# Kernel optimization log

Measured on AMD Instinct MI355X. Metric: run time of the kernel, lower is better.

The kernel has to match this reference:

```python
import jax, jax.numpy as jnp
import numpy as np

N, F, H, D, E, G = 50000, 64, 4, 64, 800000, 64
NEG_SLOPE = 0.2


def setup_inputs() -> dict:
    key = jax.random.key(0)
    ks = jax.random.split(key, 10)
    return {
        "x": jax.random.normal(ks[0], (N, F), jnp.float32),
        "mask": jax.random.uniform(ks[1], (N, F), jnp.float32),
        "edge_index": jax.random.randint(ks[2], (2, E), 0, N, jnp.int64),
        "batch_idx": jnp.sort(jax.random.randint(ks[3], (N,), 0, G, jnp.int64)),
        "W_gat": jax.random.normal(ks[4], (H * D, F), jnp.float32) * 0.05,
        "att_src": jax.random.normal(ks[5], (H, D), jnp.float32) * 0.05,
        "att_dst": jax.random.normal(ks[6], (H, D), jnp.float32) * 0.05,
        "bias_gat": jax.random.normal(ks[7], (H * D,), jnp.float32) * 0.05,
        "W_lin": jax.random.normal(ks[8], (D, H * D), jnp.float32) * 0.05,
        "b_lin": jax.random.normal(ks[9], (D,), jnp.float32) * 0.05,
    }


def reference(x, mask, edge_index, batch_idx, W_gat, att_src, att_dst, bias_gat, W_lin, b_lin):
    n = x.shape[0]
    row, col = edge_index[0], edge_index[1]

    # ---- get_mask(mask, edge_index, hops=1): scatter_add(mask[col] -> row), threshold
    m = jax.ops.segment_sum(mask[col], row, num_segments=n)
    m = (m > 0).astype(x.dtype)  # [N, F]

    # ---- GATConv(x, edge_index): add self loops (PyG default)
    loop = jnp.arange(n, dtype=edge_index.dtype)
    src = jnp.concatenate([edge_index[0], loop])  # source j
    dst = jnp.concatenate([edge_index[1], loop])  # target i

    xw = (x @ W_gat.T).reshape(n, H, D)  # per-head projection [N,H,D]
    a_s = jnp.einsum("nhd,hd->nh", xw, att_src)  # [N,H]
    a_d = jnp.einsum("nhd,hd->nh", xw, att_dst)
    e = jax.nn.leaky_relu(a_s[src] + a_d[dst], NEG_SLOPE)  # [E+N, H]

    # segment softmax over incoming edges of each destination node
    emax = jax.ops.segment_max(e, dst, num_segments=n)  # [N,H]
    ex = jnp.exp(e - emax[dst])
    denom = jax.ops.segment_sum(ex, dst, num_segments=n)
    alpha = ex / (denom[dst] + 1e-16)  # [E+N, H]

    out = jax.ops.segment_sum(alpha[:, :, None] * xw[src], dst, num_segments=n)
    out = out.reshape(n, H * D) + bias_gat  # concat heads + bias

    # ---- mask expand to heads and fuse: x = linear(x * mask)
    mexp = jnp.broadcast_to(m[:, None, :], (n, H, F)).reshape(n, H * F)
    out = (out * mexp) @ W_lin.T + b_lin  # [N, D]

    # ---- GraphSizeNorm: divide by sqrt(#nodes in each graph)
    deg = jax.ops.segment_sum(jnp.ones((n,), x.dtype), batch_idx, num_segments=G)
    inv_sqrt = jnp.where(deg > 0, deg, 1.0) ** -0.5
    out = out * inv_sqrt[batch_idx][:, None]
    return out
```

## Files before the change

kernel.cpp:

```cpp
#include <hip/hip_runtime.h>
#include <cstdint>
#include <math.h>

constexpr float NEG_SLOPE = 0.2f;

__device__ __forceinline__ float lrelu(float v) { return v > 0.0f ? v : NEG_SLOPE * v; }

__device__ __forceinline__ unsigned short f2bf(float f) {
    uint32_t u = __float_as_uint(f);
    uint32_t r = (u + 0x7fffu + ((u >> 16) & 1u)) >> 16;
    return (unsigned short)r;
}
__device__ __forceinline__ float bf2f(unsigned short v) { return __uint_as_float((uint32_t)v << 16); }
__device__ __forceinline__ float bflo(uint32_t v) { return __uint_as_float(v << 16); }
__device__ __forceinline__ float bfhi(uint32_t v) { return __uint_as_float(v & 0xffff0000u); }

typedef short bf16x8 __attribute__((ext_vector_type(8)));
typedef float f32x4 __attribute__((ext_vector_type(4)));

__global__ void k_init(const float* __restrict__ mask,
                       unsigned long long* __restrict__ mbits,
                       unsigned long long* __restrict__ magg,
                       int* __restrict__ deg, int* __restrict__ startg, int N)
{
    if (blockIdx.x == 0 && threadIdx.x < 64) startg[threadIdx.x] = N;
    int wid  = (blockIdx.x * blockDim.x + threadIdx.x) >> 6;
    int lane = threadIdx.x & 63;
    if (wid >= N) return;
    float v = mask[(size_t)wid * 64 + lane];
    unsigned long long b = __ballot(v > 0.0f);
    if (lane == 0) { mbits[wid] = b; magg[wid] = 0ULL; deg[wid] = 0; }
}

__global__ void k_edge_prep(const int* __restrict__ ei,
                            const unsigned long long* __restrict__ mbits,
                            unsigned long long* __restrict__ magg,
                            int* __restrict__ deg, int E)
{
    int e = blockIdx.x * blockDim.x + threadIdx.x;
    if (e >= E) return;
    int r = ei[e];
    int c = ei[E + e];
    unsigned long long b = mbits[c];
    if ((magg[r] & b) != b) atomicOr(magg + r, b);
    atomicAdd(deg + c, 1);
}

__launch_bounds__(256)
__global__ void k_att2(const float* __restrict__ x, const float* __restrict__ Wg,
                       const float* __restrict__ att_s, const float* __restrict__ att_d,
                       float* __restrict__ a_s, float* __restrict__ a_d, int N)
{
    __shared__ float vs_l[256];
    __shared__ float vd_l[256];
    int tid = threadIdx.x;
    {
        int h = tid >> 6, k = tid & 63;
        float s = 0.f, d = 0.f;
        for (int dd = 0; dd < 64; ++dd) {
            float w = Wg[(size_t)(h * 64 + dd) * 64 + k];
            s += w * att_s[h * 64 + dd];
            d += w * att_d[h * 64 + dd];
        }
        vs_l[tid] = s; vd_l[tid] = d;
    }
    __syncthreads();
    int i = blockIdx.x * 256 + tid;
    if (i >= N) return;
    const float4* xr = (const float4*)(x + (size_t)i * 64);
    float s0=0,s1=0,s2=0,s3=0, d0=0,d1=0,d2=0,d3=0;
    #pragma unroll
    for (int q = 0; q < 16; ++q) {
        float4 xv = xr[q];
        float4 a0 = *(const float4*)&vs_l[4*q];
        float4 a1 = *(const float4*)&vs_l[64 + 4*q];
        float4 a2 = *(const float4*)&vs_l[128 + 4*q];
        float4 a3 = *(const float4*)&vs_l[192 + 4*q];
        float4 c0 = *(const float4*)&vd_l[4*q];
        float4 c1 = *(const float4*)&vd_l[64 + 4*q];
        float4 c2 = *(const float4*)&vd_l[128 + 4*q];
        float4 c3 = *(const float4*)&vd_l[192 + 4*q];
        s0 += xv.x*a0.x + xv.y*a0.y + xv.z*a0.z + xv.w*a0.w;
        s1 += xv.x*a1.x + xv.y*a1.y + xv.z*a1.z + xv.w*a1.w;
        s2 += xv.x*a2.x + xv.y*a2.y + xv.z*a2.z + xv.w*a2.w;
        s3 += xv.x*a3.x + xv.y*a3.y + xv.z*a3.z + xv.w*a3.w;
        d0 += xv.x*c0.x + xv.y*c0.y + xv.z*c0.z + xv.w*c0.w;
        d1 += xv.x*c1.x + xv.y*c1.y + xv.z*c1.z + xv.w*c1.w;
        d2 += xv.x*c2.x + xv.y*c2.y + xv.z*c2.z + xv.w*c2.w;
        d3 += xv.x*c3.x + xv.y*c3.y + xv.z*c3.z + xv.w*c3.w;
    }
    *(float4*)&a_s[(size_t)i * 4] = make_float4(s0, s1, s2, s3);
    *(float4*)&a_d[(size_t)i * 4] = make_float4(d0, d1, d2, d3);
}

__launch_bounds__(256)
__global__ void k_gemm1m(const float* __restrict__ x, const float* __restrict__ Wg,
                         const int* __restrict__ batch_idx,
                         uint32_t* __restrict__ xwp, int* __restrict__ startg, int N)
{
    __shared__ __align__(16) uint32_t AsH[2048];
    __shared__ __align__(16) uint32_t AsL[2048];
    __shared__ __align__(16) uint32_t BsH[8192];
    const int tid = threadIdx.x;
    const int r0  = blockIdx.x * 64;

    for (int idx = tid; idx < 2048; idx += 256) {
        int r = idx >> 5, k2 = idx & 31;
        float2 v = make_float2(0.f, 0.f);
        if (r0 + r < N) v = *(const float2*)&x[(size_t)(r0 + r) * 64 + 2 * k2];
        unsigned short h0 = f2bf(v.x), h1 = f2bf(v.y);
        unsigned short l0 = f2bf(v.x - bf2f(h0)), l1 = f2bf(v.y - bf2f(h1));
        int di = (r * 32 + k2) ^ ((r & 7) << 2);
        AsH[di] = (uint32_t)h0 | ((uint32_t)h1 << 16);
        AsL[di] = (uint32_t)l0 | ((uint32_t)l1 << 16);
    }
    for (int idx = tid; idx < 8192; idx += 256) {
        int c = idx >> 5, k2 = idx & 31;
        float2 v = *(const float2*)&Wg[(size_t)c * 64 + 2 * k2];
        int di = (c * 32 + k2) ^ ((c & 7) << 2);
        BsH[di] = (uint32_t)f2bf(v.x) | ((uint32_t)f2bf(v.y) << 16);
    }
    if (tid < 64 && (r0 + tid) < N) {
        int i = r0 + tid;
        int b = batch_idx[i];
        int pb = (i > 0) ? batch_idx[i - 1] : -1;
        if (b != pb) startg[b] = i;
    }
    __syncthreads();

    const int lane = tid & 63;
    const int wv   = tid >> 6;
    const int rl   = lane & 15;
    const int kg   = lane >> 4;
    const int ct0  = (wv & 1) * 2 + (wv >> 1) * 8;
    const int swz  = (rl & 7) << 2;

    f32x4 acc[4][4];
    #pragma unroll
    for (int r = 0; r < 4; ++r)
        #pragma unroll
        for (int cs = 0; cs < 4; ++cs) acc[r][cs] = (f32x4){0.f, 0.f, 0.f, 0.f};

    #pragma unroll
    for (int ks = 0; ks < 2; ++ks) {
        bf16x8 aH[4], aL[4], bH[4];
        #pragma unroll
        for (int r = 0; r < 4; ++r) {
            int ui = (((r * 16 + rl) * 32) + ks * 16 + kg * 4) ^ swz;
            aH[r] = *(const bf16x8*)&AsH[ui];
            aL[r] = *(const bf16x8*)&AsL[ui];
        }
        #pragma unroll
        for (int cs = 0; cs < 4; ++cs) {
            int ct = ct0 + (cs & 1) + (cs >> 1) * 4;
            int ui = (((ct * 16 + rl) * 32) + ks * 16 + kg * 4) ^ swz;
            bH[cs] = *(const bf16x8*)&BsH[ui];
        }
        #pragma unroll
        for (int r = 0; r < 4; ++r)
            #pragma unroll
            for (int cs = 0; cs < 4; ++cs) {
                acc[r][cs] = __builtin_amdgcn_mfma_f32_16x16x32_bf16(aH[r], bH[cs], acc[r][cs], 0, 0, 0);
                acc[r][cs] = __builtin_amdgcn_mfma_f32_16x16x32_bf16(aL[r], bH[cs], acc[r][cs], 0, 0, 0);
            }
    }

    #pragma unroll
    for (int r = 0; r < 4; ++r) {
        #pragma unroll
        for (int reg = 0; reg < 4; ++reg) {
            int row = r0 + r * 16 + kg * 4 + reg;
            if (row < N) {
                #pragma unroll
                for (int p = 0; p < 2; ++p) {
                    int c_lo = (ct0 + p) * 16 + rl;
                    int wrd  = ((c_lo >> 7) << 6) | (c_lo & 63);
                    uint32_t lo = f2bf(acc[r][p][reg]);
                    uint32_t hi = f2bf(acc[r][p + 2][reg]);
                    xwp[(size_t)row * 128 + wrd] = lo | (hi << 16);
                }
            }
        }
    }
}

__global__ void k_scan1(const int* __restrict__ deg, int* __restrict__ off,
                        int* __restrict__ bsum, int N)
{
    __shared__ int s[256];
    int t = threadIdx.x;
    int i = blockIdx.x * 256 + t;
    int v = (i < N) ? deg[i] : 0;
    s[t] = v; __syncthreads();
    for (int o = 1; o < 256; o <<= 1) {
        int u = (t >= o) ? s[t - o] : 0;
        __syncthreads();
        s[t] += u;
        __syncthreads();
    }
    int incl = s[t];
    if (i < N) off[i] = incl - v;
    if (t == 255) bsum[blockIdx.x] = incl;
}

__global__ void k_scan2(const int* __restrict__ bsum, int* __restrict__ bpre,
                        int* __restrict__ off, const int* __restrict__ startg,
                        float* __restrict__ invs, int NB, int N)
{
    __shared__ int s[256];
    int t = threadIdx.x;
    int v = (t < NB) ? bsum[t] : 0;
    s[t] = v; __syncthreads();
    for (int o = 1; o < 256; o <<= 1) {
        int u = (t >= o) ? s[t - o] : 0;
        __syncthreads();
        s[t] += u;
        __syncthreads();
    }
    if (t < NB) bpre[t] = s[t] - v;
    if (t == 255) off[N] = s[255];
    if (t < 64) {
        int st = startg[t];
        int en = N;
        for (int g2 = t + 1; g2 < 64; ++g2) en = min(en, startg[g2]);
        int d = en - st;
        float dv = (d > 0) ? (float)d : 1.0f;
        invs[t] = 1.0f / sqrtf(dv);
    }
}

__global__ void k_scan3(int* __restrict__ off, int* __restrict__ cursor,
                        const int* __restrict__ bpre, int N)
{
    int i = blockIdx.x * blockDim.x + threadIdx.x;
    if (i >= N) return;
    int v = off[i] + bpre[blockIdx.x];
    off[i] = v;
    cursor[i] = v;
}

__global__ void k_fill(const int* __restrict__ ei, int* __restrict__ cursor,
                       int* __restrict__ csr, int E)
{
    int e = blockIdx.x * blockDim.x + threadIdx.x;
    if (e >= E) return;
    int r = ei[e];
    int c = ei[E + e];
    int pos = atomicAdd(cursor + c, 1);
    csr[pos] = r;
}

__launch_bounds__(256)
__global__ void k_main5(const uint32_t* __restrict__ xwp,
                        const float* __restrict__ a_s,
                        const float* __restrict__ a_d,
                        const int* __restrict__ off,
                        const int* __restrict__ csr,
                        const unsigned long long* __restrict__ magg,
                        const float* __restrict__ bias,
                        float* __restrict__ tb, int N)
{
    __shared__ __align__(16) uint32_t su[4][64];
    __shared__ float2 e01s[4][64];
    __shared__ float2 e23s[4][64];

    const int lane = threadIdx.x & 63;
    const int wv   = threadIdx.x >> 6;
    const int wid  = blockIdx.x * 4 + wv;
    const int nw   = gridDim.x * 4;
    const int hp   = lane >> 5;
    const int d0   = (lane & 31) * 2;

    const uint2* xw2 = (const uint2*)xwp;
    const float2 bsL = *(const float2*)&bias[hp * 128 + d0];
    const float2 bsH = *(const float2*)&bias[hp * 128 + 64 + d0];
    const float2* ep = hp ? e23s[wv] : e01s[wv];

    for (int i = wid; i < N; i += nw) {
        const int beg = off[i], end = off[i + 1];
        const float4 adv = *(const float4*)(a_d + (size_t)i * 4);
        const float4 asv = *(const float4*)(a_s + (size_t)i * 4);
        const float ex0 = __expf(lrelu(asv.x + adv.x));
        const float ex1 = __expf(lrelu(asv.y + adv.y));
        const float ex2 = __expf(lrelu(asv.z + adv.z));
        const float ex3 = __expf(lrelu(asv.w + adv.w));

        const uint2 sv = xw2[(size_t)i * 64 + lane];
        const float wls = hp ? ex2 : ex0;
        const float whs = hp ? ex3 : ex1;
        float accL0 = wls * bflo(sv.x), accH0 = whs * bfhi(sv.x);
        float accL1 = wls * bflo(sv.y), accH1 = whs * bfhi(sv.y);
        float s0 = 0.f, s1 = 0.f, s2 = 0.f, s3 = 0.f;

        for (int kc = beg; kc < end; kc += 64) {
            const int cnt = min(64, end - kc);
            uint32_t sreg = 0; float e0 = 0.f, e1 = 0.f, e2 = 0.f, e3 = 0.f;
            if (lane < cnt) {
                sreg = csr[kc + lane];
                const float4 g = *(const float4*)(a_s + (size_t)sreg * 4);
                e0 = __expf(lrelu(g.x + adv.x));
                e1 = __expf(lrelu(g.y + adv.y));
                e2 = __expf(lrelu(g.z + adv.z));
                e3 = __expf(lrelu(g.w + adv.w));
            }
            s0 += e0; s1 += e1; s2 += e2; s3 += e3;
            su[wv][lane]   = sreg;
            e01s[wv][lane] = make_float2(e0, e1);
            e23s[wv][lane] = make_float2(e2, e3);

            int j = 0;
            for (; j + 4 <= cnt; j += 4) {
                uint4 sq = *(const uint4*)&su[wv][j];
                float2 wA = ep[j], wB = ep[j+1], wC = ep[j+2], wD = ep[j+3];
                uint2 vA = xw2[(size_t)sq.x * 64 + lane];
                uint2 vB = xw2[(size_t)sq.y * 64 + lane];
                uint2 vC = xw2[(size_t)sq.z * 64 + lane];
                uint2 vD = xw2[(size_t)sq.w * 64 + lane];
                accL0 += wA.x * bflo(vA.x); accH0 += wA.y * bfhi(vA.x);
                accL1 += wA.x * bflo(vA.y); accH1 += wA.y * bfhi(vA.y);
                accL0 += wB.x * bflo(vB.x); accH0 += wB.y * bfhi(vB.x);
                accL1 += wB.x * bflo(vB.y); accH1 += wB.y * bfhi(vB.y);
                accL0 += wC.x * bflo(vC.x); accH0 += wC.y * bfhi(vC.x);
                accL1 += wC.x * bflo(vC.y); accH1 += wC.y * bfhi(vC.y);
                accL0 += wD.x * bflo(vD.x); accH0 += wD.y * bfhi(vD.x);
                accL1 += wD.x * bflo(vD.y); accH1 += wD.y * bfhi(vD.y);
            }
            for (; j < cnt; ++j) {
                uint32_t s = su[wv][j];
                float2 wE = ep[j];
                uint2 v = xw2[(size_t)s * 64 + lane];
                accL0 += wE.x * bflo(v.x); accH0 += wE.y * bfhi(v.x);
                accL1 += wE.x * bflo(v.y); accH1 += wE.y * bfhi(v.y);
            }
        }
        #pragma unroll
        for (int o = 1; o < 64; o <<= 1) {
            s0 += __shfl_xor(s0, o); s1 += __shfl_xor(s1, o);
            s2 += __shfl_xor(s2, o); s3 += __shfl_xor(s3, o);
        }
        s0 += ex0; s1 += ex1; s2 += ex2; s3 += ex3;
        const float slo = hp ? s2 : s0;
        const float shi = hp ? s3 : s1;
        const float rlo = 1.0f / (slo + 1e-16f);
        const float rhi = 1.0f / (shi + 1e-16f);

        const unsigned long long mb = magg[i];
        const float m0 = (float)((mb >> d0) & 1ULL);
        const float m1 = (float)((mb >> (d0 + 1)) & 1ULL);
        float2 oL = make_float2((accL0 * rlo + bsL.x) * m0, (accL1 * rlo + bsL.y) * m1);
        float2 oH = make_float2((accH0 * rhi + bsH.x) * m0, (accH1 * rhi + bsH.y) * m1);
        *(float2*)&tb[(size_t)i * 256 + hp * 128 + d0]      = oL;
        *(float2*)&tb[(size_t)i * 256 + hp * 128 + 64 + d0] = oH;
    }
}

__launch_bounds__(256)
__global__ void k_gemm2m(const float* __restrict__ tb, const float* __restrict__ Wl,
                         const float* __restrict__ bl,
                         const int* __restrict__ batch_idx, const float* __restrict__ invs,
                         float* __restrict__ out, int N)
{
    __shared__ __align__(16) uint32_t AH[2048];
    __shared__ __align__(16) uint32_t AL[2048];
    __shared__ __align__(16) uint32_t BH[2048];
    __shared__ __align__(16) uint32_t BL[2048];
    const int tid = threadIdx.x;
    const int r0  = blockIdx.x * 64;
    const int lane = tid & 63;
    const int wv   = tid >> 6;
    const int rl   = lane & 15;
    const int kg   = lane >> 4;
    const int swz  = (rl & 7) << 2;

    f32x4 acc[4];
    #pragma unroll
    for (int r = 0; r < 4; ++r) acc[r] = (f32x4){0.f, 0.f, 0.f, 0.f};

    for (int kc = 0; kc < 4; ++kc) {
        if (kc) __syncthreads();
        for (int idx = tid; idx < 2048; idx += 256) {
            int r = idx >> 5, k2 = idx & 31;
            float2 v = make_float2(0.f, 0.f);
            if (r0 + r < N) v = *(const float2*)&tb[(size_t)(r0 + r) * 256 + kc * 64 + 2 * k2];
            unsigned short h0 = f2bf(v.x), h1 = f2bf(v.y);
            unsigned short l0 = f2bf(v.x - bf2f(h0)), l1 = f2bf(v.y - bf2f(h1));
            int di = (r * 32 + k2) ^ ((r & 7) << 2);
            AH[di] = (uint32_t)h0 | ((uint32_t)h1 << 16);
            AL[di] = (uint32_t)l0 | ((uint32_t)l1 << 16);
        }
        for (int idx = tid; idx < 2048; idx += 256) {
            int c = idx >> 5, k2 = idx & 31;
            float2 v = *(const float2*)&Wl[(size_t)c * 256 + kc * 64 + 2 * k2];
            unsigned short h0 = f2bf(v.x), h1 = f2bf(v.y);
            unsigned short l0 = f2bf(v.x - bf2f(h0)), l1 = f2bf(v.y - bf2f(h1));
            int di = (c * 32 + k2) ^ ((c & 7) << 2);
            BH[di] = (uint32_t)h0 | ((uint32_t)h1 << 16);
            BL[di] = (uint32_t)l0 | ((uint32_t)l1 << 16);
        }
        __syncthreads();

        #pragma unroll
        for (int ks = 0; ks < 2; ++ks) {
            int uib = ((wv * 16 + rl) * 32 + ks * 16 + kg * 4) ^ swz;
            bf16x8 bHf = *(const bf16x8*)&BH[uib];
            bf16x8 bLf = *(const bf16x8*)&BL[uib];
            #pragma unroll
            for (int r = 0; r < 4; ++r) {
                int ui = ((r * 16 + rl) * 32 + ks * 16 + kg * 4) ^ swz;
                bf16x8 aHf = *(const bf16x8*)&AH[ui];
                bf16x8 aLf = *(const bf16x8*)&AL[ui];
                acc[r] = __builtin_amdgcn_mfma_f32_16x16x32_bf16(aHf, bHf, acc[r], 0, 0, 0);
                acc[r] = __builtin_amdgcn_mfma_f32_16x16x32_bf16(aHf, bLf, acc[r], 0, 0, 0);
                acc[r] = __builtin_amdgcn_mfma_f32_16x16x32_bf16(aLf, bHf, acc[r], 0, 0, 0);
            }
        }
    }

    const int col = wv * 16 + rl;
    const float blc = bl[col];
    #pragma unroll
    for (int r = 0; r < 4; ++r) {
        #pragma unroll
        for (int reg = 0; reg < 4; ++reg) {
            int row = r0 + r * 16 + kg * 4 + reg;
            if (row < N) {
                float sc = invs[batch_idx[row]];
                out[(size_t)row * 64 + col] = (acc[r][reg] + blc) * sc;
            }
        }
    }
}

extern "C" void kernel_launch(void* const* d_in, const int* in_sizes, int n_in,
                              void* d_out, int out_size, void* d_ws, size_t ws_size,
                              hipStream_t stream)
{
    const float* x      = (const float*)d_in[0];
    const float* mask   = (const float*)d_in[1];
    const int*   ei     = (const int*)d_in[2];
    const int*   batch  = (const int*)d_in[3];
    const float* Wg     = (const float*)d_in[4];
    const float* att_s  = (const float*)d_in[5];
    const float* att_d  = (const float*)d_in[6];
    const float* bias_g = (const float*)d_in[7];
    const float* Wl     = (const float*)d_in[8];
    const float* bl     = (const float*)d_in[9];
    float* out = (float*)d_out;

    const int N = in_sizes[0] / 64;
    const int E = in_sizes[2] / 2;

    char* w = (char*)d_ws;
    auto alloc = [&](size_t bytes) { char* p = w; w += (bytes + 255) & ~(size_t)255; return p; };
    uint32_t* xwp  = (uint32_t*)alloc((size_t)N * 128 * 4);
    float* tbuf  = (float*)alloc((size_t)N * 256 * 4);
    float* a_s   = (float*)alloc((size_t)N * 4 * 4);
    float* a_d   = (float*)alloc((size_t)N * 4 * 4);
    unsigned long long* mbits = (unsigned long long*)alloc((size_t)N * 8);
    unsigned long long* magg  = (unsigned long long*)alloc((size_t)N * 8);
    int* deg    = (int*)alloc((size_t)N * 4);
    int* off    = (int*)alloc((size_t)(N + 1) * 4);
    int* cursor = (int*)alloc((size_t)N * 4);
    int* csr    = (int*)alloc((size_t)E * 4);
    int* bsum   = (int*)alloc(256 * 4);
    int* bpre   = (int*)alloc(256 * 4);
    int* startg = (int*)alloc(64 * 4);
    float* invs = (float*)alloc(64 * 4);

    int nbN4  = (N + 3) / 4;
    int nb256 = (N + 255) / 256;

    k_init<<<nbN4, 256, 0, stream>>>(mask, mbits, magg, deg, startg, N);
    k_edge_prep<<<(E + 255) / 256, 256, 0, stream>>>(ei, mbits, magg, deg, E);
    k_att2<<<nb256, 256, 0, stream>>>(x, Wg, att_s, att_d, a_s, a_d, N);
    k_gemm1m<<<(N + 63) / 64, 256, 0, stream>>>(x, Wg, batch, xwp, startg, N);
    k_scan1<<<nb256, 256, 0, stream>>>(deg, off, bsum, N);
    k_scan2<<<1, 256, 0, stream>>>(bsum, bpre, off, startg, invs, nb256, N);
    k_scan3<<<nb256, 256, 0, stream>>>(off, cursor, bpre, N);
    k_fill<<<(E + 255) / 256, 256, 0, stream>>>(ei, cursor, csr, E);
    k_main5<<<2048, 256, 0, stream>>>(xwp, a_s, a_d, off, csr, magg, bias_g, tbuf, N);
    k_gemm2m<<<(N + 63) / 64, 256, 0, stream>>>(tbuf, Wl, bl, batch, invs, out, N);
}
```

Before: 259.3 us.

## Merge three-pass scan into one kernel, move mask OR into fill, unroll gather by 8

Replaces the three-kernel prefix scan over node degrees with a single 1024-thread block in which each thread serially scans a chunk. This removes two launches and one pass over the offsets. The mask-bit OR aggregation moves from the degree-counting kernel into the CSR fill kernel, so the edge list is read one fewer time. The aggregation kernel adds an 8-wide unrolled gather loop to get more loads in flight, at the cost of extra registers. The single-block scan leaves most of the GPU idle and its per-thread chunk reads are uncoalesced.

```diff
diff --git a/kernel.cpp b/kernel.cpp
--- a/kernel.cpp
+++ b/kernel.cpp
@@ -32,18 +32,11 @@
     if (lane == 0) { mbits[wid] = b; magg[wid] = 0ULL; deg[wid] = 0; }
 }
 
-__global__ void k_edge_prep(const int* __restrict__ ei,
-                            const unsigned long long* __restrict__ mbits,
-                            unsigned long long* __restrict__ magg,
-                            int* __restrict__ deg, int E)
+__global__ void k_deg(const int* __restrict__ ei, int* __restrict__ deg, int E)
 {
     int e = blockIdx.x * blockDim.x + threadIdx.x;
     if (e >= E) return;
-    int r = ei[e];
-    int c = ei[E + e];
-    unsigned long long b = mbits[c];
-    if ((magg[r] & b) != b) atomicOr(magg + r, b);
-    atomicAdd(deg + c, 1);
+    atomicAdd(deg + ei[E + e], 1);
 }
 
 __launch_bounds__(256)
@@ -184,41 +177,38 @@
     }
 }
 
-__global__ void k_scan1(const int* __restrict__ deg, int* __restrict__ off,
-                        int* __restrict__ bsum, int N)
-{
-    __shared__ int s[256];
-    int t = threadIdx.x;
-    int i = blockIdx.x * 256 + t;
-    int v = (i < N) ? deg[i] : 0;
-    s[t] = v; __syncthreads();
-    for (int o = 1; o < 256; o <<= 1) {
-        int u = (t >= o) ? s[t - o] : 0;
+__launch_bounds__(1024)
+__global__ void k_scan(const int* __restrict__ deg, int* __restrict__ off,
+                       int* __restrict__ cursor, const int* __restrict__ startg,
+                       float* __restrict__ invs, int N)
+{
+    __shared__ int psum[1024];
+    const int t = threadIdx.x;
+    const int per = (N + 1023) / 1024;
+    const int b0 = t * per;
+    int s = 0;
+    for (int k = 0; k < per; ++k) {
+        int i = b0 + k;
+        if (i < N) s += deg[i];
+    }
+    psum[t] = s;
+    __syncthreads();
+    for (int o = 1; o < 1024; o <<= 1) {
+        int u = (t >= o) ? psum[t - o] : 0;
         __syncthreads();
-        s[t] += u;
+        psum[t] += u;
         __syncthreads();
     }
-    int incl = s[t];
-    if (i < N) off[i] = incl - v;
-    if (t == 255) bsum[blockIdx.x] = incl;
-}
-
-__global__ void k_scan2(const int* __restrict__ bsum, int* __restrict__ bpre,
-                        int* __restrict__ off, const int* __restrict__ startg,
-                        float* __restrict__ invs, int NB, int N)
-{
-    __shared__ int s[256];
-    int t = threadIdx.x;
-    int v = (t < NB) ? bsum[t] : 0;
-    s[t] = v; __syncthreads();
-    for (int o = 1; o < 256; o <<= 1) {
-        int u = (t >= o) ? s[t - o] : 0;
-        __syncthreads();
-        s[t] += u;
-        __syncthreads();
-    }
-    if (t < NB) bpre[t] = s[t] - v;
-    if (t == 255) off[N] = s[255];
+    int run = psum[t] - s;
+    for (int k = 0; k < per; ++k) {
+        int i = b0 + k;
+        if (i < N) {
+            off[i] = run;
+            cursor[i] = run;
+            run += deg[i];
+        }
+    }
+    if (t == 1023) off[N] = psum[1023];
     if (t < 64) {
         int st = startg[t];
         int en = N;
@@ -229,29 +219,23 @@
     }
 }
 
-__global__ void k_scan3(int* __restrict__ off, int* __restrict__ cursor,
-                        const int* __restrict__ bpre, int N)
-{
-    int i = blockIdx.x * blockDim.x + threadIdx.x;
-    if (i >= N) return;
-    int v = off[i] + bpre[blockIdx.x];
-    off[i] = v;
-    cursor[i] = v;
-}
-
 __global__ void k_fill(const int* __restrict__ ei, int* __restrict__ cursor,
-                       int* __restrict__ csr, int E)
+                       int* __restrict__ csr,
+                       const unsigned long long* __restrict__ mbits,
+                       unsigned long long* __restrict__ magg, int E)
 {
     int e = blockIdx.x * blockDim.x + threadIdx.x;
     if (e >= E) return;
     int r = ei[e];
     int c = ei[E + e];
+    unsigned long long b = mbits[c];
+    if ((magg[r] & b) != b) atomicOr(magg + r, b);
     int pos = atomicAdd(cursor + c, 1);
     csr[pos] = r;
 }
 
 __launch_bounds__(256)
-__global__ void k_main5(const uint32_t* __restrict__ xwp,
+__global__ void k_main6(const uint32_t* __restrict__ xwp,
                         const float* __restrict__ a_s,
                         const float* __restrict__ a_d,
                         const int* __restrict__ off,
@@ -261,8 +245,8 @@
                         float* __restrict__ tb, int N)
 {
     __shared__ __align__(16) uint32_t su[4][64];
-    __shared__ float2 e01s[4][64];
-    __shared__ float2 e23s[4][64];
+    __shared__ __align__(16) float2 e01s[4][64];
+    __shared__ __align__(16) float2 e23s[4][64];
 
     const int lane = threadIdx.x & 63;
     const int wv   = threadIdx.x >> 6;
@@ -309,6 +293,36 @@
             e23s[wv][lane] = make_float2(e2, e3);
 
             int j = 0;
+            for (; j + 8 <= cnt; j += 8) {
+                uint4 sq0 = *(const uint4*)&su[wv][j];
+                uint4 sq1 = *(const uint4*)&su[wv][j + 4];
+                float2 w0 = ep[j],   w1 = ep[j+1], w2 = ep[j+2], w3 = ep[j+3];
+                float2 w4 = ep[j+4], w5 = ep[j+5], w6 = ep[j+6], w7 = ep[j+7];
+                uint2 v0 = xw2[(size_t)sq0.x * 64 + lane];
+                uint2 v1 = xw2[(size_t)sq0.y * 64 + lane];
+                uint2 v2 = xw2[(size_t)sq0.z * 64 + lane];
+                uint2 v3 = xw2[(size_t)sq0.w * 64 + lane];
+                uint2 v4 = xw2[(size_t)sq1.x * 64 + lane];
+                uint2 v5 = xw2[(size_t)sq1.y * 64 + lane];
+                uint2 v6 = xw2[(size_t)sq1.z * 64 + lane];
+                uint2 v7 = xw2[(size_t)sq1.w * 64 + lane];
+                accL0 += w0.x * bflo(v0.x); accH0 += w0.y * bfhi(v0.x);
+                accL1 += w0.x * bflo(v0.y); accH1 += w0.y * bfhi(v0.y);
+                accL0 += w1.x * bflo(v1.x); accH0 += w1.y * bfhi(v1.x);
+                accL1 += w1.x * bflo(v1.y); accH1 += w1.y * bfhi(v1.y);
+                accL0 += w2.x * bflo(v2.x); accH0 += w2.y * bfhi(v2.x);
+                accL1 += w2.x * bflo(v2.y); accH1 += w2.y * bfhi(v2.y);
+                accL0 += w3.x * bflo(v3.x); accH0 += w3.y * bfhi(v3.x);
+                accL1 += w3.x * bflo(v3.y); accH1 += w3.y * bfhi(v3.y);
+                accL0 += w4.x * bflo(v4.x); accH0 += w4.y * bfhi(v4.x);
+                accL1 += w4.x * bflo(v4.y); accH1 += w4.y * bfhi(v4.y);
+                accL0 += w5.x * bflo(v5.x); accH0 += w5.y * bfhi(v5.x);
+                accL1 += w5.x * bflo(v5.y); accH1 += w5.y * bfhi(v5.y);
+                accL0 += w6.x * bflo(v6.x); accH0 += w6.y * bfhi(v6.x);
+                accL1 += w6.x * bflo(v6.y); accH1 += w6.y * bfhi(v6.y);
+                accL0 += w7.x * bflo(v7.x); accH0 += w7.y * bfhi(v7.x);
+                accL1 += w7.x * bflo(v7.y); accH1 += w7.y * bfhi(v7.y);
+            }
             for (; j + 4 <= cnt; j += 4) {
                 uint4 sq = *(const uint4*)&su[wv][j];
                 float2 wA = ep[j], wB = ep[j+1], wC = ep[j+2], wD = ep[j+3];
@@ -462,8 +476,6 @@
     int* off    = (int*)alloc((size_t)(N + 1) * 4);
     int* cursor = (int*)alloc((size_t)N * 4);
     int* csr    = (int*)alloc((size_t)E * 4);
-    int* bsum   = (int*)alloc(256 * 4);
-    int* bpre   = (int*)alloc(256 * 4);
     int* startg = (int*)alloc(64 * 4);
     float* invs = (float*)alloc(64 * 4);
 
@@ -471,13 +483,11 @@
     int nb256 = (N + 255) / 256;
 
     k_init<<<nbN4, 256, 0, stream>>>(mask, mbits, magg, deg, startg, N);
-    k_edge_prep<<<(E + 255) / 256, 256, 0, stream>>>(ei, mbits, magg, deg, E);
+    k_deg<<<(E + 255) / 256, 256, 0, stream>>>(ei, deg, E);
     k_att2<<<nb256, 256, 0, stream>>>(x, Wg, att_s, att_d, a_s, a_d, N);
     k_gemm1m<<<(N + 63) / 64, 256, 0, stream>>>(x, Wg, batch, xwp, startg, N);
-    k_scan1<<<nb256, 256, 0, stream>>>(deg, off, bsum, N);
-    k_scan2<<<1, 256, 0, stream>>>(bsum, bpre, off, startg, invs, nb256, N);
-    k_scan3<<<nb256, 256, 0, stream>>>(off, cursor, bpre, N);
-    k_fill<<<(E + 255) / 256, 256, 0, stream>>>(ei, cursor, csr, E);
-    k_main5<<<2048, 256, 0, stream>>>(xwp, a_s, a_d, off, csr, magg, bias_g, tbuf, N);
+    k_scan<<<1, 1024, 0, stream>>>(deg, off, cursor, startg, invs, N);
+    k_fill<<<(E + 255) / 256, 256, 0, stream>>>(ei, cursor, csr, mbits, magg, E);
+    k_main6<<<2048, 256, 0, stream>>>(xwp, a_s, a_d, off, csr, magg, bias_g, tbuf, N);
     k_gemm2m<<<(N + 63) / 64, 256, 0, stream>>>(tbuf, Wl, bl, batch, invs, out, N);
 }
```

Result: slower. 354.0 us (+36.5%).
